# Optimization experiments

Measured on AMD Instinct MI355X. Metric: run time of the kernel, lower is better.

Reference implementation:

```python
import jax, jax.numpy as jnp
import numpy as np
import math

N_HEAD = 12


def setup_inputs() -> dict:
    key = jax.random.key(0)
    k1, k2, k3 = jax.random.split(key, 3)
    B, T, C = 4, 2048, 768
    x = jax.random.normal(k1, (B, T, C), dtype=jnp.float32)
    W = jax.random.normal(k2, (C, 3 * C), dtype=jnp.float32) * 0.02
    b = jax.random.normal(k3, (3 * C,), dtype=jnp.float32) * 0.02
    return {"x": x, "W": W, "b": b}


def reference(x, W, b):
    B, T, C = x.shape
    H = N_HEAD
    d = C // H
    qkv = x @ W + b                                # [B,T,3C]
    q, k, v = jnp.split(qkv, 3, axis=-1)           # each [B,T,C]
    q = q.reshape(B, T, H, d).transpose(0, 2, 1, 3)  # [B,H,T,d]
    k = k.reshape(B, T, H, d).transpose(0, 2, 1, 3)
    v = v.reshape(B, T, H, d).transpose(0, 2, 1, 3)
    # NOTE: source multiplies by sqrt(d) (not divides) -- faithful reproduction.
    att = jnp.einsum('bhqd,bhkd->bhqk', q, k) * (1.0 * math.sqrt(d))
    causal = jnp.tril(jnp.ones((T, T), dtype=bool))  # [T,T]
    att = jnp.where(causal[None, None, :, :], att, -jnp.inf)
    att = jax.nn.softmax(att, axis=-1)
    y = jnp.einsum('bhqk,bhkd->bhqd', att, v)      # [B,H,T,d]
    y = y.transpose(0, 2, 1, 3).reshape(B, T, C)   # [B,T,C]
    return y
```

## Files before the change

### kernel.cpp

```cpp
#include <hip/hip_runtime.h>
#include <math.h>

#define B_ 4
#define T_ 2048
#define C_ 768
#define H_ 12
#define D_ 64
#define N3C (3*C_)
#define BH_ (B_*H_)
#define QSCALE 11.5415603f
#define PPS 72

typedef float f32x4 __attribute__((ext_vector_type(4)));
typedef _Float16 f16x8 __attribute__((ext_vector_type(8)));
typedef unsigned short ushort_t;

__device__ __forceinline__ void async16(const void* g, void* l) {
    __builtin_amdgcn_global_load_lds(
        (const __attribute__((address_space(1))) unsigned int*)(g),
        (__attribute__((address_space(3))) unsigned int*)(l),
        16, 0, 0);
}

__device__ __forceinline__ unsigned pk_f16(float a, float b) {
    __fp16 r2[2];
    *(__fp16 __attribute__((ext_vector_type(2)))*)r2 = __builtin_amdgcn_cvt_pkrtz(a, b);
    return *(unsigned*)r2;
}

__global__ __launch_bounds__(256) void conv_x(const float* __restrict__ x,
                                              _Float16* __restrict__ Xh)
{
    int idx = blockIdx.x * 256 + threadIdx.x;
    const float4 a = *reinterpret_cast<const float4*>(&x[(size_t)idx * 8]);
    const float4 b = *reinterpret_cast<const float4*>(&x[(size_t)idx * 8 + 4]);
    f16x8 o = {(_Float16)a.x, (_Float16)a.y, (_Float16)a.z, (_Float16)a.w,
               (_Float16)b.x, (_Float16)b.y, (_Float16)b.z, (_Float16)b.w};
    *reinterpret_cast<f16x8*>(&Xh[(size_t)idx * 8]) = o;
}

__global__ __launch_bounds__(256) void conv_w(const float* __restrict__ W,
                                              _Float16* __restrict__ Wh)
{
    __shared__ float tile[64][65];
    int n0 = blockIdx.x * 64, k0 = blockIdx.y * 64;
    int tid = threadIdx.x;
    #pragma unroll
    for (int t = 0; t < 16; ++t) {
        int c = t * 256 + tid;
        int kr = c >> 6, nc = c & 63;
        tile[kr][nc] = W[(size_t)(k0 + kr) * N3C + n0 + nc];
    }
    __syncthreads();
    #pragma unroll
    for (int t = 0; t < 16; ++t) {
        int c = t * 256 + tid;
        int nr = c >> 6, kc = c & 63;
        Wh[(size_t)(n0 + nr) * C_ + k0 + kc] = (_Float16)tile[kc][nr];
    }
}

__global__ __launch_bounds__(256) void qkv_gemm(const _Float16* __restrict__ Xh,
                                                const _Float16* __restrict__ Wh,
                                                const float* __restrict__ bias,
                                                _Float16* __restrict__ Qf,
                                                _Float16* __restrict__ Kf,
                                                _Float16* __restrict__ Vt)
{
    __shared__ __align__(16) ushort_t As[128 * 64];
    __shared__ __align__(16) ushort_t Bs[128 * 64];

    int tid = threadIdx.x, lane = tid & 63, w = tid >> 6;
    int wm = w >> 1, wn = w & 1;
    int l15 = lane & 15, l4 = lane >> 4;
    int srow = lane >> 3;
    int scol = (((lane & 7) ^ srow)) << 3;

    int wg = blockIdx.x;
    int l = (wg & 7) * 144 + (wg >> 3);
    int mt = l / 18, nt = l % 18;
    int row0 = mt * 128, col0 = nt * 128;

    f32x4 acc[4][4];
    #pragma unroll
    for (int i = 0; i < 4; ++i)
        #pragma unroll
        for (int j = 0; j < 4; ++j)
            acc[i][j] = f32x4{0.f, 0.f, 0.f, 0.f};

    const char* AsC = (const char*)As;
    const char* BsC = (const char*)Bs;

    for (int k0 = 0; k0 < C_; k0 += 64) {
        __syncthreads();
        #pragma unroll
        for (int j = 0; j < 4; ++j) {
            int rowb = w * 32 + j * 8;
            async16(Xh + (size_t)(row0 + rowb + srow) * C_ + k0 + scol, &As[rowb * 64]);
            async16(Wh + (size_t)(col0 + rowb + srow) * C_ + k0 + scol, &Bs[rowb * 64]);
        }
        __syncthreads();

        #pragma unroll
        for (int kk = 0; kk < 2; ++kk) {
            f16x8 af[4], bfr[4];
            #pragma unroll
            for (int m = 0; m < 4; ++m) {
                int r = wm * 64 + m * 16 + l15;
                af[m] = *reinterpret_cast<const f16x8*>(AsC + r * 128 + ((kk * 64 + l4 * 16) ^ ((r & 7) << 4)));
            }
            #pragma unroll
            for (int n = 0; n < 4; ++n) {
                int r = wn * 64 + n * 16 + l15;
                bfr[n] = *reinterpret_cast<const f16x8*>(BsC + r * 128 + ((kk * 64 + l4 * 16) ^ ((r & 7) << 4)));
            }
            #pragma unroll
            for (int m = 0; m < 4; ++m)
                #pragma unroll
                for (int n = 0; n < 4; ++n)
                    acc[m][n] = __builtin_amdgcn_mfma_f32_16x16x32_f16(af[m], bfr[n], acc[m][n], 0, 0, 0);
        }
    }

    #pragma unroll
    for (int n = 0; n < 4; ++n) {
        int gcol = col0 + wn * 64 + n * 16 + l15;
        int p    = gcol / C_;
        int rem  = gcol - p * C_;
        int h    = rem >> 6, d = rem & 63;
        float bv = bias[gcol];
        #pragma unroll
        for (int m = 0; m < 4; ++m) {
            #pragma unroll
            for (int r = 0; r < 4; ++r) {
                int grow = row0 + wm * 64 + m * 16 + l4 * 4 + r;
                int b = grow >> 11, t = grow & (T_ - 1);
                int bh = b * H_ + h;
                float v = acc[m][n][r] + bv;
                if (p == 0) {
                    Qf[((size_t)bh * T_ + t) * D_ + d] = (_Float16)(v * QSCALE);
                } else if (p == 1) {
                    Kf[((size_t)bh * T_ + t) * D_ + d] = (_Float16)v;
                } else {
                    Vt[((size_t)bh * D_ + d) * T_ + t] = (_Float16)v;
                }
            }
        }
    }
}

__device__ const unsigned char ITEM_QT[24] = {15,15,7,14,14,13,13,6,12,12,11,11,5,10,10,9,9,4,8,8,3,2,1,0};
__device__ const unsigned char ITEM_CH[24] = { 0, 1,0, 0, 1, 0, 1,0, 0, 1, 0, 1,0, 0, 1,0,1,0,0,1,0,0,0,0};

__global__ __launch_bounds__(256) void attn(const _Float16* __restrict__ Qf,
                                            const _Float16* __restrict__ Kf,
                                            const _Float16* __restrict__ Vt,
                                            float* __restrict__ out,
                                            float* __restrict__ Op,
                                            float* __restrict__ ML)
{
    __shared__ __align__(16) char smem[41984];
    ushort_t* lds = (ushort_t*)smem;

    int tid = threadIdx.x, lane = tid & 63, w = tid >> 6;
    int l15 = lane & 15, l4 = lane >> 4;
    int bid = blockIdx.x;
    int rank = bid / BH_;
    int bh = bid % BH_;
    int qt = ITEM_QT[rank];
    int ch = ITEM_CH[rank];
    int b = bh / H_, h = bh % H_;
    int q0 = qt * 128;

    int it0 = (qt < 8 || ch == 0) ? 0 : (qt + 1);
    int it1 = (qt >= 8 && ch == 0) ? (qt + 1) : (2 * qt + 2);

    f16x8 qf[2][2];
    #pragma unroll
    for (int qs = 0; qs < 2; ++qs) {
        int q = q0 + w * 32 + qs * 16 + l15;
        const _Float16* ph = Qf + ((size_t)bh * T_ + q) * D_;
        qf[qs][0] = *reinterpret_cast<const f16x8*>(ph + l4 * 8);
        qf[qs][1] = *reinterpret_cast<const f16x8*>(ph + 32 + l4 * 8);
    }

    f32x4 yacc[2][4];
    #pragma unroll
    for (int qs = 0; qs < 2; ++qs)
        #pragma unroll
        for (int dt = 0; dt < 4; ++dt)
            yacc[qs][dt] = f32x4{0.f, 0.f, 0.f, 0.f};
    float m_run[2] = {-INFINITY, -INFINITY};
    float l_run[2] = {0.f, 0.f};

    int srow = lane >> 3;
    int scol = ((lane & 7) ^ srow) << 3;
    ushort_t* Pw = lds + 16384 + w * (16 * PPS);
    const size_t kbase = (size_t)bh * T_;
    const size_t vbase = (size_t)bh * D_;

    {
        int k00 = it0 * 64;
        #pragma unroll
        for (int j = 0; j < 2; ++j) {
            int row = (w * 2 + j) * 8 + srow;
            ushort_t* dK = lds + (w * 2 + j) * 512;
            async16(Kf + (kbase + k00 + row) * D_ + scol, dK);
            async16(Vt + (vbase + row) * T_ + k00 + scol, dK + 4096);
        }
    }
    __syncthreads();

    int cur = 0;
    for (int it = it0; it < it1; ++it) {
        int k0 = it * 64;
        int nxt = cur ^ 1;
        if (it + 1 < it1) {
            int k0n = k0 + 64;
            #pragma unroll
            for (int j = 0; j < 2; ++j) {
                int row = (w * 2 + j) * 8 + srow;
                ushort_t* dK = lds + nxt * 8192 + (w * 2 + j) * 512;
                async16(Kf + (kbase + k0n + row) * D_ + scol, dK);
                async16(Vt + (vbase + row) * T_ + k0n + scol, dK + 4096);
            }
        }

        if (k0 <= q0 + w * 32 + 31) {
            const char* KHc = (const char*)(lds + cur * 8192);
            const char* VSc = KHc + 8192;
            f16x8 pa[2][2];

            #pragma unroll
            for (int qs = 0; qs < 2; ++qs) {
                f32x4 sa[4];
                #pragma unroll
                for (int i = 0; i < 4; ++i) sa[i] = f32x4{0.f, 0.f, 0.f, 0.f};

                __builtin_amdgcn_s_setprio(1);
                #pragma unroll
                for (int kt = 0; kt < 4; ++kt) {
                    int krow = kt * 16 + l15;
                    int swz = (krow & 7) << 4;
                    #pragma unroll
                    for (int dh = 0; dh < 2; ++dh) {
                        f16x8 kf = *reinterpret_cast<const f16x8*>(KHc + krow * 128 + ((dh * 64 + l4 * 16) ^ swz));
                        sa[kt] = __builtin_amdgcn_mfma_f32_16x16x32_f16(kf, qf[qs][dh], sa[kt], 0, 0, 0);
                    }
                }
                __builtin_amdgcn_s_setprio(0);

                if (it >= 2 * qt) {
                    int qg = q0 + w * 32 + qs * 16 + l15;
                    #pragma unroll
                    for (int kt = 0; kt < 4; ++kt)
                        #pragma unroll
                        for (int r = 0; r < 4; ++r)
                            if (k0 + kt * 16 + l4 * 4 + r > qg) sa[kt][r] = -INFINITY;
                }

                float mx = sa[0][0];
                #pragma unroll
                for (int kt = 0; kt < 4; ++kt)
                    #pragma unroll
                    for (int r = 0; r < 4; ++r) mx = fmaxf(mx, sa[kt][r]);
                mx = fmaxf(mx, __shfl_xor(mx, 16));
                mx = fmaxf(mx, __shfl_xor(mx, 32));

                float mn;
                if (__all(mx <= m_run[qs] + 8.0f)) {
                    mn = m_run[qs];
                } else {
                    mn = fmaxf(m_run[qs], mx);
                    float sc = exp2f(m_run[qs] - mn);
                    m_run[qs] = mn;
                    l_run[qs] *= sc;
                    #pragma unroll
                    for (int dt = 0; dt < 4; ++dt) yacc[qs][dt] *= sc;
                }

                float p[4][4];
                float rs = 0.f;
                #pragma unroll
                for (int kt = 0; kt < 4; ++kt)
                    #pragma unroll
                    for (int r = 0; r < 4; ++r) {
                        p[kt][r] = exp2f(sa[kt][r] - mn);
                        rs += p[kt][r];
                    }
                rs += __shfl_xor(rs, 16);
                rs += __shfl_xor(rs, 32);
                l_run[qs] += rs;

                int pb = l15 * PPS + l4 * 4;
                #pragma unroll
                for (int kt = 0; kt < 4; ++kt) {
                    *reinterpret_cast<unsigned*>(Pw + pb + kt * 16) = pk_f16(p[kt][0], p[kt][1]);
                    *reinterpret_cast<unsigned*>(Pw + pb + kt * 16 + 2) = pk_f16(p[kt][2], p[kt][3]);
                }
                pa[qs][0] = *reinterpret_cast<const f16x8*>(Pw + l15 * PPS + l4 * 8);
                pa[qs][1] = *reinterpret_cast<const f16x8*>(Pw + l15 * PPS + 32 + l4 * 8);
            }

            __builtin_amdgcn_s_setprio(1);
            #pragma unroll
            for (int dt = 0; dt < 4; ++dt) {
                int vrow = dt * 16 + l15;
                int vswz = (vrow & 7) << 4;
                #pragma unroll
                for (int kk = 0; kk < 2; ++kk) {
                    f16x8 vf = *reinterpret_cast<const f16x8*>(VSc + vrow * 128 + ((kk * 64 + l4 * 16) ^ vswz));
                    yacc[0][dt] = __builtin_amdgcn_mfma_f32_16x16x32_f16(vf, pa[0][kk], yacc[0][dt], 0, 0, 0);
                    yacc[1][dt] = __builtin_amdgcn_mfma_f32_16x16x32_f16(vf, pa[1][kk], yacc[1][dt], 0, 0, 0);
                }
            }
            __builtin_amdgcn_s_setprio(0);
        }
        __syncthreads();
        cur = nxt;
    }

    float* ot = (float*)smem;
    if (qt < 8) {
        #pragma unroll
        for (int qs = 0; qs < 2; ++qs) {
            float inv = 1.0f / l_run[qs];
            int rq = w * 32 + qs * 16 + l15;
            #pragma unroll
            for (int dt = 0; dt < 4; ++dt)
                #pragma unroll
                for (int r = 0; r < 4; ++r)
                    ot[rq * 68 + dt * 16 + l4 * 4 + r] = yacc[qs][dt][r] * inv;
        }
        __syncthreads();
        int rr = tid >> 1, c0 = (tid & 1) * 32;
        size_t ob = ((size_t)(b * T_ + q0 + rr)) * C_ + h * D_ + c0;
        #pragma unroll
        for (int u = 0; u < 8; ++u) {
            float4 v = *reinterpret_cast<const float4*>(&ot[rr * 68 + c0 + u * 4]);
            *reinterpret_cast<float4*>(&out[ob + u * 4]) = v;
        }
    } else {
        #pragma unroll
        for (int qs = 0; qs < 2; ++qs) {
            int rq = w * 32 + qs * 16 + l15;
            #pragma unroll
            for (int dt = 0; dt < 4; ++dt)
                #pragma unroll
                for (int r = 0; r < 4; ++r)
                    ot[rq * 68 + dt * 16 + l4 * 4 + r] = yacc[qs][dt][r];
        }
        if (l4 == 0) {
            float* mlp = ML + (((size_t)bh * 8 + (qt - 8)) * 2 + ch) * 256;
            #pragma unroll
            for (int qs = 0; qs < 2; ++qs) {
                int ql = w * 32 + qs * 16 + l15;
                mlp[ql] = m_run[qs];
                mlp[128 + ql] = l_run[qs];
            }
        }
        __syncthreads();
        int rr = tid >> 1, c0 = (tid & 1) * 32;
        float* dst = Op + (((size_t)bh * 8 + (qt - 8)) * 2 + ch) * 8192 + rr * 64 + c0;
        #pragma unroll
        for (int u = 0; u < 8; ++u) {
            float4 v = *reinterpret_cast<const float4*>(&ot[rr * 68 + c0 + u * 4]);
            *reinterpret_cast<float4*>(&dst[u * 4]) = v;
        }
    }
}

__global__ __launch_bounds__(256) void merge(const float* __restrict__ Op,
                                             const float* __restrict__ ML,
                                             float* __restrict__ out)
{
    int gid = blockIdx.x * 256 + threadIdx.x;
    int row = gid >> 4, seg = gid & 15;
    int q = row & 127, qt8 = (row >> 7) & 7, bh = row >> 10;

    size_t mbase = ((size_t)bh * 8 + qt8) * 2 * 256;
    float m1 = ML[mbase + q],       l1 = ML[mbase + 128 + q];
    float m2 = ML[mbase + 256 + q], l2 = ML[mbase + 256 + 128 + q];
    float m = fmaxf(m1, m2);
    float a1 = exp2f(m1 - m), a2 = exp2f(m2 - m);
    float inv = 1.0f / (l1 * a1 + l2 * a2);

    size_t obase = ((size_t)bh * 8 + qt8) * 2 * 8192 + q * 64 + seg * 4;
    float4 o1 = *reinterpret_cast<const float4*>(&Op[obase]);
    float4 o2 = *reinterpret_cast<const float4*>(&Op[obase + 8192]);
    float4 r;
    r.x = (o1.x * a1 + o2.x * a2) * inv;
    r.y = (o1.y * a1 + o2.y * a2) * inv;
    r.z = (o1.z * a1 + o2.z * a2) * inv;
    r.w = (o1.w * a1 + o2.w * a2) * inv;

    int b = bh / H_, h = bh % H_;
    int t = (qt8 + 8) * 128 + q;
    *reinterpret_cast<float4*>(&out[((size_t)(b * T_ + t)) * C_ + h * D_ + seg * 4]) = r;
}

extern "C" void kernel_launch(void* const* d_in, const int* in_sizes, int n_in,
                              void* d_out, int out_size, void* d_ws, size_t ws_size,
                              hipStream_t stream)
{
    const float* x    = (const float*)d_in[0];
    const float* W    = (const float*)d_in[1];
    const float* bias = (const float*)d_in[2];

    const size_t per = (size_t)BH_ * T_ * D_;
    _Float16* Qf = (_Float16*)d_ws;
    _Float16* Kf = Qf + per;
    _Float16* Vt = Kf + per;
    _Float16* Xh = Vt + per;
    _Float16* Wh = Xh + (size_t)8192 * C_;
    float*    Op = (float*)(Wh + (size_t)N3C * C_);
    float*    ML = Op + (size_t)48 * 8 * 2 * 8192;

    conv_x<<<dim3((8192 * 768 / 8) / 256), 256, 0, stream>>>(x, Xh);
    conv_w<<<dim3(N3C / 64, C_ / 64), 256, 0, stream>>>(W, Wh);
    qkv_gemm<<<dim3(64 * 18), 256, 0, stream>>>(Xh, Wh, bias, Qf, Kf, Vt);
    attn<<<dim3(24 * BH_), 256, 0, stream>>>(Qf, Kf, Vt, (float*)d_out, Op, ML);
    merge<<<dim3(49152 * 16 / 256), 256, 0, stream>>>(Op, ML, (float*)d_out);
}
```

Measured before the change: 152.3 us.

## Fold running max into score init and compute row sums via MFMA

Initializes the QK accumulator with the negated running max so the subtraction is absorbed into the MFMA, and replaces the per-lane row-sum reduction (adds plus cross-lane shuffles) with an extra MFMA against a ones vector. The P staging buffer switches from padded rows to an XOR-swizzled layout, which shrinks LDS use. It also starts the running max at a finite value instead of -inf. This trades VALU and shuffle work for two extra MFMAs per tile, and the rounded f16 P now feeds the denominator.

```diff
diff --git a/kernel.cpp b/kernel.cpp
--- a/kernel.cpp
+++ b/kernel.cpp
@@ -9,7 +9,7 @@
 #define N3C (3*C_)
 #define BH_ (B_*H_)
 #define QSCALE 11.5415603f
-#define PPS 72
+#define M_INIT -63.0f
 
 typedef float f32x4 __attribute__((ext_vector_type(4)));
 typedef _Float16 f16x8 __attribute__((ext_vector_type(8)));
@@ -159,7 +159,7 @@
                                             float* __restrict__ Op,
                                             float* __restrict__ ML)
 {
-    __shared__ __align__(16) char smem[41984];
+    __shared__ __align__(16) char smem[40960];
     ushort_t* lds = (ushort_t*)smem;
 
     int tid = threadIdx.x, lane = tid & 63, w = tid >> 6;
@@ -184,18 +184,25 @@
         qf[qs][1] = *reinterpret_cast<const f16x8*>(ph + 32 + l4 * 8);
     }
 
+    f16x8 ones;
+    #pragma unroll
+    for (int j = 0; j < 8; ++j) ones[j] = (_Float16)1.0f;
+
     f32x4 yacc[2][4];
-    #pragma unroll
-    for (int qs = 0; qs < 2; ++qs)
+    f32x4 yl[2];
+    #pragma unroll
+    for (int qs = 0; qs < 2; ++qs) {
         #pragma unroll
         for (int dt = 0; dt < 4; ++dt)
             yacc[qs][dt] = f32x4{0.f, 0.f, 0.f, 0.f};
-    float m_run[2] = {-INFINITY, -INFINITY};
-    float l_run[2] = {0.f, 0.f};
+        yl[qs] = f32x4{0.f, 0.f, 0.f, 0.f};
+    }
+    float m_run[2] = {M_INIT, M_INIT};
 
     int srow = lane >> 3;
     int scol = ((lane & 7) ^ srow) << 3;
-    ushort_t* Pw = lds + 16384 + w * (16 * PPS);
+    char* PwB = (char*)(lds + 16384 + w * 1024);
+    int pswz = (l15 & 7) << 4;
     const size_t kbase = (size_t)bh * T_;
     const size_t vbase = (size_t)bh * D_;
 
@@ -233,9 +240,10 @@
 
             #pragma unroll
             for (int qs = 0; qs < 2; ++qs) {
+                float bias = -m_run[qs];
                 f32x4 sa[4];
                 #pragma unroll
-                for (int i = 0; i < 4; ++i) sa[i] = f32x4{0.f, 0.f, 0.f, 0.f};
+                for (int i = 0; i < 4; ++i) sa[i] = f32x4{bias, bias, bias, bias};
 
                 __builtin_amdgcn_s_setprio(1);
                 #pragma unroll
@@ -267,39 +275,37 @@
                 mx = fmaxf(mx, __shfl_xor(mx, 16));
                 mx = fmaxf(mx, __shfl_xor(mx, 32));
 
-                float mn;
-                if (__all(mx <= m_run[qs] + 8.0f)) {
-                    mn = m_run[qs];
+                float p[4][4];
+                if (__all(mx <= 8.0f)) {
+                    #pragma unroll
+                    for (int kt = 0; kt < 4; ++kt)
+                        #pragma unroll
+                        for (int r = 0; r < 4; ++r)
+                            p[kt][r] = exp2f(sa[kt][r]);
                 } else {
-                    mn = fmaxf(m_run[qs], mx);
-                    float sc = exp2f(m_run[qs] - mn);
-                    m_run[qs] = mn;
-                    l_run[qs] *= sc;
+                    float step = fmaxf(mx, 0.0f);
+                    float sc = exp2f(-step);
+                    m_run[qs] += step;
+                    yl[qs] *= sc;
                     #pragma unroll
                     for (int dt = 0; dt < 4; ++dt) yacc[qs][dt] *= sc;
-                }
-
-                float p[4][4];
-                float rs = 0.f;
-                #pragma unroll
-                for (int kt = 0; kt < 4; ++kt)
-                    #pragma unroll
-                    for (int r = 0; r < 4; ++r) {
-                        p[kt][r] = exp2f(sa[kt][r] - mn);
-                        rs += p[kt][r];
-                    }
-                rs += __shfl_xor(rs, 16);
-                rs += __shfl_xor(rs, 32);
-                l_run[qs] += rs;
-
-                int pb = l15 * PPS + l4 * 4;
+                    #pragma unroll
+                    for (int kt = 0; kt < 4; ++kt)
+                        #pragma unroll
+                        for (int r = 0; r < 4; ++r)
+                            p[kt][r] = exp2f(sa[kt][r] - step);
+                }
+
                 #pragma unroll
                 for (int kt = 0; kt < 4; ++kt) {
-                    *reinterpret_cast<unsigned*>(Pw + pb + kt * 16) = pk_f16(p[kt][0], p[kt][1]);
-                    *reinterpret_cast<unsigned*>(Pw + pb + kt * 16 + 2) = pk_f16(p[kt][2], p[kt][3]);
-                }
-                pa[qs][0] = *reinterpret_cast<const f16x8*>(Pw + l15 * PPS + l4 * 8);
-                pa[qs][1] = *reinterpret_cast<const f16x8*>(Pw + l15 * PPS + 32 + l4 * 8);
+                    uint2 pw;
+                    pw.x = pk_f16(p[kt][0], p[kt][1]);
+                    pw.y = pk_f16(p[kt][2], p[kt][3]);
+                    int off = (l15 * 128 + kt * 32 + l4 * 8) ^ pswz;
+                    *reinterpret_cast<uint2*>(PwB + off) = pw;
+                }
+                pa[qs][0] = *reinterpret_cast<const f16x8*>(PwB + ((l15 * 128 + l4 * 16) ^ pswz));
+                pa[qs][1] = *reinterpret_cast<const f16x8*>(PwB + ((l15 * 128 + 64 + l4 * 16) ^ pswz));
             }
 
             __builtin_amdgcn_s_setprio(1);
@@ -314,6 +320,11 @@
                     yacc[1][dt] = __builtin_amdgcn_mfma_f32_16x16x32_f16(vf, pa[1][kk], yacc[1][dt], 0, 0, 0);
                 }
             }
+            #pragma unroll
+            for (int kk = 0; kk < 2; ++kk) {
+                yl[0] = __builtin_amdgcn_mfma_f32_16x16x32_f16(ones, pa[0][kk], yl[0], 0, 0, 0);
+                yl[1] = __builtin_amdgcn_mfma_f32_16x16x32_f16(ones, pa[1][kk], yl[1], 0, 0, 0);
+            }
             __builtin_amdgcn_s_setprio(0);
         }
         __syncthreads();
@@ -324,7 +335,7 @@
     if (qt < 8) {
         #pragma unroll
         for (int qs = 0; qs < 2; ++qs) {
-            float inv = 1.0f / l_run[qs];
+            float inv = 1.0f / yl[qs][0];
             int rq = w * 32 + qs * 16 + l15;
             #pragma unroll
             for (int dt = 0; dt < 4; ++dt)
@@ -356,7 +367,7 @@
             for (int qs = 0; qs < 2; ++qs) {
                 int ql = w * 32 + qs * 16 + l15;
                 mlp[ql] = m_run[qs];
-                mlp[128 + ql] = l_run[qs];
+                mlp[128 + ql] = yl[qs][0];
             }
         }
         __syncthreads();
```

After: 160.1 us. 1.05x slower.
